# Optimization experiments

Hardware: AMD Instinct MI355X
Metric: run time of the kernel (lower is better)

Reference implementation:

```python
import jax, jax.numpy as jnp
import numpy as np

IN_CAP_NUM = 1024
IN_CAP_DIM = 64
OUT_CAP_NUM = 32
OUT_CAP_DIM = 64
BATCH = 64
NUM_ITER = 3


def squash(t):
    # t: [..., d]; scale = |t|^2 / (1+|t|^2) / |t|
    sq = jnp.sum(t * t, axis=-1, keepdims=True)
    scale = sq / (1.0 + sq) / jnp.sqrt(sq)
    return scale * t


def setup_inputs() -> dict:
    key = jax.random.key(0)
    k1, k2 = jax.random.split(key)
    x = jax.random.normal(k1, (IN_CAP_NUM, BATCH, IN_CAP_DIM), dtype=jnp.float32)
    route_w = 0.1 * jax.random.normal(
        k2, (OUT_CAP_NUM, IN_CAP_NUM, IN_CAP_DIM, OUT_CAP_DIM), dtype=jnp.float32)
    return {"x": x, "route_w": route_w}


def reference(x, route_w):
    # u[o,i,b,e] = sum_d x[i,b,d] * route_w[o,i,d,e]  (torch broadcast matmul)
    u = jnp.einsum('ibd,oide->oibe', x, route_w)  # [O, I, B, E]
    O = route_w.shape[0]
    b = jnp.zeros((O, 1, 1, 1), dtype=u.dtype)
    v = None
    for it in range(NUM_ITER):
        c = jax.nn.softmax(b, axis=0)                 # coupling over out caps
        s = jnp.sum(c * u, axis=1)                    # [O, B, E]
        v = squash(s)                                 # [O, B, E]
        if it < NUM_ITER - 1:
            # agreement: [O, I, B, 1]
            b = b + jnp.sum(u * v[:, None, :, :], axis=-1, keepdims=True)
    return v
```

## Files before the change

kernel.cpp:

```cpp
#include <hip/hip_runtime.h>
#include <hip/hip_bf16.h>
#include <stdint.h>


#define IC 1024
#define OC 32
#define DD 64
#define EE 64
#define BB 64

typedef __attribute__((ext_vector_type(8))) short short8;
typedef __attribute__((ext_vector_type(16))) float f32x16;

__device__ __forceinline__ unsigned short f2bf(float f) {
    unsigned int u = __float_as_uint(f);
    u = (u + 0x7FFFu + ((u >> 16) & 1u)) >> 16;
    return (unsigned short)u;
}
__device__ __forceinline__ unsigned int pk2(float a, float b) {
    return (unsigned int)f2bf(a) | ((unsigned int)f2bf(b) << 16);
}

template<bool UNIFORM>
__global__ __launch_bounds__(256)
void gemm_s_kernel(const float* __restrict__ x,
                   const float* __restrict__ w,
                   const float* __restrict__ cbuf,
                   float* __restrict__ s_out)
{
    __shared__ unsigned short xs[64 * 68];
    __shared__ unsigned short wT[64 * 68];
    const int t = threadIdx.x;
    const int o = blockIdx.y;
    const int chunk = blockIdx.x;
    const int lane = t & 63;
    const int wv = t >> 6;
    const int bh = wv & 1, eh = wv >> 1;
    const int seg = t & 7;
    const int rrow = t >> 3;

    f32x16 acc = (f32x16)0.0f;

    for (int ii = 0; ii < 32; ++ii) {
        const int i = chunk * 32 + ii;
        __syncthreads();
        for (int hlf = 0; hlf < 2; ++hlf) {
            const int b = rrow + hlf * 32;
            const float* xp = x + (((size_t)i) * BB + b) * DD + seg * 8;
            const float4 xa = *(const float4*)xp;
            const float4 xb = *(const float4*)(xp + 4);
            float c;
            if (UNIFORM) c = 1.0f / 32.0f;
            else         c = cbuf[(((size_t)o) * IC + i) * BB + b];
            uint2* dst = (uint2*)&xs[b * 68 + seg * 8];
            dst[0] = make_uint2(pk2(xa.x * c, xa.y * c), pk2(xa.z * c, xa.w * c));
            dst[1] = make_uint2(pk2(xb.x * c, xb.y * c), pk2(xb.z * c, xb.w * c));
        }
        {
            const int d0 = rrow * 2;
            const float* wp = w + ((((size_t)o) * IC + i) * DD + d0) * EE + seg * 8;
            const float4 a0 = *(const float4*)(wp);
            const float4 a1 = *(const float4*)(wp + 4);
            const float4 b0 = *(const float4*)(wp + EE);
            const float4 b1 = *(const float4*)(wp + EE + 4);
            const float r0[8] = {a0.x, a0.y, a0.z, a0.w, a1.x, a1.y, a1.z, a1.w};
            const float r1[8] = {b0.x, b0.y, b0.z, b0.w, b1.x, b1.y, b1.z, b1.w};
            #pragma unroll
            for (int j = 0; j < 8; ++j) {
                const int e = seg * 8 + j;
                *(unsigned int*)&wT[e * 68 + d0] = pk2(r0[j], r1[j]);
            }
        }
        __syncthreads();
        #pragma unroll
        for (int kk = 0; kk < 4; ++kk) {
            const int k0 = kk * 16 + (lane >> 5) * 8;
            const int ar = bh * 32 + (lane & 31);
            const int br = eh * 32 + (lane & 31);
            uint2 alo = *(const uint2*)&xs[ar * 68 + k0];
            uint2 ahi = *(const uint2*)&xs[ar * 68 + k0 + 4];
            uint2 blo = *(const uint2*)&wT[br * 68 + k0];
            uint2 bhi = *(const uint2*)&wT[br * 68 + k0 + 4];
            union { uint4 u; short8 s; } au, bu;
            au.u = make_uint4(alo.x, alo.y, ahi.x, ahi.y);
            bu.u = make_uint4(blo.x, blo.y, bhi.x, bhi.y);
            acc = __builtin_amdgcn_mfma_f32_32x32x16_bf16(au.s, bu.s, acc, 0, 0, 0);
        }
    }
    #pragma unroll
    for (int r = 0; r < 16; ++r) {
        const int gb = bh * 32 + (r & 3) + 8 * (r >> 2) + 4 * (lane >> 5);
        const int ge = eh * 32 + (lane & 31);
        atomicAdd(&s_out[(((size_t)o) * BB + gb) * EE + ge], acc[r]);
    }
}

template<bool FIRST>
__global__ __launch_bounds__(256)
void logits_kernel(const float* __restrict__ x,
                   const float* __restrict__ w,
                   const unsigned short* __restrict__ vbuf,
                   const float* __restrict__ bprev,
                   float* __restrict__ bout,
                   float* __restrict__ cbuf)
{
    __shared__ float xT[64 * 65];
    __shared__ unsigned short wls[64 * 68];
    __shared__ unsigned short vls[64 * 68];
    __shared__ float Lp[OC][2][BB];
    const int t = threadIdx.x;
    const int i = blockIdx.x;
    const int lane = t & 63;
    const int wv = t >> 6;
    const int dh = wv & 1, bh = wv >> 1;
    const int seg = t & 7;
    const int rrow = t >> 3;

    for (int hlf = 0; hlf < 2; ++hlf) {
        const int b = rrow + hlf * 32;
        const float* xp = x + (((size_t)i) * BB + b) * DD + seg * 8;
        const float4 xa = *(const float4*)xp;
        const float4 xb = *(const float4*)(xp + 4);
        const float xv[8] = {xa.x, xa.y, xa.z, xa.w, xb.x, xb.y, xb.z, xb.w};
        #pragma unroll
        for (int j = 0; j < 8; ++j)
            xT[(seg * 8 + j) * 65 + b] = xv[j];
    }

    for (int o = 0; o < OC; ++o) {
        __syncthreads();
        for (int hlf = 0; hlf < 2; ++hlf) {
            const int d = rrow + hlf * 32;
            const float* wp = w + ((((size_t)o) * IC + i) * DD + d) * EE + seg * 8;
            const float4 wa = *(const float4*)wp;
            const float4 wb = *(const float4*)(wp + 4);
            uint2* dst = (uint2*)&wls[d * 68 + seg * 8];
            dst[0] = make_uint2(pk2(wa.x, wa.y), pk2(wa.z, wa.w));
            dst[1] = make_uint2(pk2(wb.x, wb.y), pk2(wb.z, wb.w));
            const int b = d;
            const uint4 vr = *(const uint4*)(vbuf + (((size_t)o) * BB + b) * EE + seg * 8);
            uint2* vdst = (uint2*)&vls[b * 68 + seg * 8];
            vdst[0] = make_uint2(vr.x, vr.y);
            vdst[1] = make_uint2(vr.z, vr.w);
        }
        __syncthreads();
        f32x16 acc = (f32x16)0.0f;
        #pragma unroll
        for (int kk = 0; kk < 4; ++kk) {
            const int k0 = kk * 16 + (lane >> 5) * 8;
            const int dr = dh * 32 + (lane & 31);
            const int br = bh * 32 + (lane & 31);
            uint2 alo = *(const uint2*)&wls[dr * 68 + k0];
            uint2 ahi = *(const uint2*)&wls[dr * 68 + k0 + 4];
            uint2 blo = *(const uint2*)&vls[br * 68 + k0];
            uint2 bhi = *(const uint2*)&vls[br * 68 + k0 + 4];
            union { uint4 u; short8 s; } au, bu;
            au.u = make_uint4(alo.x, alo.y, ahi.x, ahi.y);
            bu.u = make_uint4(blo.x, blo.y, bhi.x, bhi.y);
            acc = __builtin_amdgcn_mfma_f32_32x32x16_bf16(au.s, bu.s, acc, 0, 0, 0);
        }
        float partial = 0.f;
        const int bcol = bh * 32 + (lane & 31);
        #pragma unroll
        for (int r = 0; r < 16; ++r) {
            const int d = dh * 32 + (r & 3) + 8 * (r >> 2) + 4 * (lane >> 5);
            partial += xT[d * 65 + bcol] * acc[r];
        }
        partial += __shfl_xor(partial, 32);
        if (lane < 32) Lp[o][dh][bcol] = partial;
    }
    __syncthreads();
    if (t < BB) {
        const int b = t;
        float lt[OC];
        float m = -1e30f;
        #pragma unroll
        for (int o = 0; o < OC; ++o) {
            float L = Lp[o][0][b] + Lp[o][1][b];
            if (!FIRST) L += bprev[(((size_t)o) * IC + i) * BB + b];
            if (FIRST)  bout[(((size_t)o) * IC + i) * BB + b] = L;
            lt[o] = L;
            m = fmaxf(m, L);
        }
        float Z = 0.f;
        #pragma unroll
        for (int o = 0; o < OC; ++o) { lt[o] = __expf(lt[o] - m); Z += lt[o]; }
        const float rZ = 1.0f / Z;
        #pragma unroll
        for (int o = 0; o < OC; ++o)
            cbuf[(((size_t)o) * IC + i) * BB + b] = lt[o] * rZ;
    }
}

template<bool TOBF>
__global__ __launch_bounds__(256)
void squash_kernel(const float* __restrict__ s, void* __restrict__ vout)
{
    const int o = blockIdx.x;
    const int lane = threadIdx.x & 63;
    const int wv = threadIdx.x >> 6;
    for (int b = wv; b < BB; b += 4) {
        const float val = s[(((size_t)o) * BB + b) * EE + lane];
        float sq = val * val;
        #pragma unroll
        for (int off = 1; off < 64; off <<= 1)
            sq += __shfl_xor(sq, off);
        const float r = sqrtf(sq);
        const float scale = r / (1.0f + sq);
        const size_t idx = (((size_t)o) * BB + b) * EE + lane;
        if (TOBF) ((unsigned short*)vout)[idx] = f2bf(val * scale);
        else      ((float*)vout)[idx] = val * scale;
    }
}

extern "C" void kernel_launch(void* const* d_in, const int* in_sizes, int n_in,
                              void* d_out, int out_size, void* d_ws, size_t ws_size,
                              hipStream_t stream)
{
    const float* x = (const float*)d_in[0];
    const float* w = (const float*)d_in[1];
    float* out = (float*)d_out;

    char* ws = (char*)d_ws;
    float*          s_buf = (float*)ws;
    unsigned short* vbuf  = (unsigned short*)(ws + 524288);
    float*          b1    = (float*)(ws + 524288 + 262144);
    float*          cbuf  = (float*)(ws + 524288 + 262144 + 8388608);

    const dim3 gridG(32, 32), blk(256);

    hipMemsetAsync(s_buf, 0, 524288, stream);
    gemm_s_kernel<true><<<gridG, blk, 0, stream>>>(x, w, nullptr, s_buf);
    squash_kernel<true><<<32, 256, 0, stream>>>(s_buf, vbuf);
    logits_kernel<true><<<1024, 256, 0, stream>>>(x, w, vbuf, nullptr, b1, cbuf);
    hipMemsetAsync(s_buf, 0, 524288, stream);
    gemm_s_kernel<false><<<gridG, blk, 0, stream>>>(x, w, cbuf, s_buf);
    squash_kernel<true><<<32, 256, 0, stream>>>(s_buf, vbuf);
    logits_kernel<false><<<1024, 256, 0, stream>>>(x, w, vbuf, b1, nullptr, cbuf);
    hipMemsetAsync(s_buf, 0, 524288, stream);
    gemm_s_kernel<false><<<gridG, blk, 0, stream>>>(x, w, cbuf, s_buf);
    squash_kernel<false><<<32, 256, 0, stream>>>(s_buf, out);
}
```

Measured before the change: 1.193 ms.

## Materialize u once in fp16 and reuse it across routing iterations

```diff
diff --git a/kernel.cpp b/kernel.cpp
--- a/kernel.cpp
+++ b/kernel.cpp
@@ -1,5 +1,4 @@
 #include <hip/hip_runtime.h>
-#include <hip/hip_bf16.h>
 #include <stdint.h>
 
 
@@ -11,6 +10,7 @@
 
 typedef __attribute__((ext_vector_type(8))) short short8;
 typedef __attribute__((ext_vector_type(16))) float f32x16;
+typedef _Float16 half8 __attribute__((ext_vector_type(8)));
 
 __device__ __forceinline__ unsigned short f2bf(float f) {
     unsigned int u = __float_as_uint(f);
@@ -21,11 +21,10 @@
     return (unsigned int)f2bf(a) | ((unsigned int)f2bf(b) << 16);
 }
 
-template<bool UNIFORM>
-__global__ __launch_bounds__(256)
-void gemm_s_kernel(const float* __restrict__ x,
+__global__ __launch_bounds__(256)
+void u_gemm_kernel(const float* __restrict__ x,
                    const float* __restrict__ w,
-                   const float* __restrict__ cbuf,
+                   _Float16* __restrict__ u,
                    float* __restrict__ s_out)
 {
     __shared__ unsigned short xs[64 * 68];
@@ -39,7 +38,7 @@
     const int seg = t & 7;
     const int rrow = t >> 3;
 
-    f32x16 acc = (f32x16)0.0f;
+    f32x16 stot = (f32x16)0.0f;
 
     for (int ii = 0; ii < 32; ++ii) {
         const int i = chunk * 32 + ii;
@@ -49,12 +48,9 @@
             const float* xp = x + (((size_t)i) * BB + b) * DD + seg * 8;
             const float4 xa = *(const float4*)xp;
             const float4 xb = *(const float4*)(xp + 4);
-            float c;
-            if (UNIFORM) c = 1.0f / 32.0f;
-            else         c = cbuf[(((size_t)o) * IC + i) * BB + b];
             uint2* dst = (uint2*)&xs[b * 68 + seg * 8];
-            dst[0] = make_uint2(pk2(xa.x * c, xa.y * c), pk2(xa.z * c, xa.w * c));
-            dst[1] = make_uint2(pk2(xb.x * c, xb.y * c), pk2(xb.z * c, xb.w * c));
+            dst[0] = make_uint2(pk2(xa.x, xa.y), pk2(xa.z, xa.w));
+            dst[1] = make_uint2(pk2(xb.x, xb.y), pk2(xb.z, xb.w));
         }
         {
             const int d0 = rrow * 2;
@@ -72,6 +68,7 @@
             }
         }
         __syncthreads();
+        f32x16 acc = (f32x16)0.0f;
         #pragma unroll
         for (int kk = 0; kk < 4; ++kk) {
             const int k0 = kk * 16 + (lane >> 5) * 8;
@@ -81,104 +78,69 @@
             uint2 ahi = *(const uint2*)&xs[ar * 68 + k0 + 4];
             uint2 blo = *(const uint2*)&wT[br * 68 + k0];
             uint2 bhi = *(const uint2*)&wT[br * 68 + k0 + 4];
-            union { uint4 u; short8 s; } au, bu;
-            au.u = make_uint4(alo.x, alo.y, ahi.x, ahi.y);
-            bu.u = make_uint4(blo.x, blo.y, bhi.x, bhi.y);
+            union { uint4 q; short8 s; } au, bu;
+            au.q = make_uint4(alo.x, alo.y, ahi.x, ahi.y);
+            bu.q = make_uint4(blo.x, blo.y, bhi.x, bhi.y);
             acc = __builtin_amdgcn_mfma_f32_32x32x16_bf16(au.s, bu.s, acc, 0, 0, 0);
+        }
+        _Float16* ub = u + ((((size_t)o) * IC + i) * BB) * EE;
+        #pragma unroll
+        for (int r = 0; r < 16; ++r) {
+            const int gb = bh * 32 + (r & 3) + 8 * (r >> 2) + 4 * (lane >> 5);
+            const int ge = eh * 32 + (lane & 31);
+            ub[gb * EE + ge] = (_Float16)acc[r];
+            stot[r] += acc[r];
         }
     }
     #pragma unroll
     for (int r = 0; r < 16; ++r) {
         const int gb = bh * 32 + (r & 3) + 8 * (r >> 2) + 4 * (lane >> 5);
         const int ge = eh * 32 + (lane & 31);
-        atomicAdd(&s_out[(((size_t)o) * BB + gb) * EE + ge], acc[r]);
+        atomicAdd(&s_out[(((size_t)o) * BB + gb) * EE + ge], stot[r] * (1.0f / 32.0f));
     }
 }
 
 template<bool FIRST>
 __global__ __launch_bounds__(256)
-void logits_kernel(const float* __restrict__ x,
-                   const float* __restrict__ w,
-                   const unsigned short* __restrict__ vbuf,
+void logits_kernel(const _Float16* __restrict__ u,
+                   const float* __restrict__ v,
                    const float* __restrict__ bprev,
                    float* __restrict__ bout,
                    float* __restrict__ cbuf)
 {
-    __shared__ float xT[64 * 65];
-    __shared__ unsigned short wls[64 * 68];
-    __shared__ unsigned short vls[64 * 68];
-    __shared__ float Lp[OC][2][BB];
+    __shared__ float Lp[OC][BB];
     const int t = threadIdx.x;
     const int i = blockIdx.x;
-    const int lane = t & 63;
-    const int wv = t >> 6;
-    const int dh = wv & 1, bh = wv >> 1;
-    const int seg = t & 7;
-    const int rrow = t >> 3;
-
-    for (int hlf = 0; hlf < 2; ++hlf) {
-        const int b = rrow + hlf * 32;
-        const float* xp = x + (((size_t)i) * BB + b) * DD + seg * 8;
-        const float4 xa = *(const float4*)xp;
-        const float4 xb = *(const float4*)(xp + 4);
-        const float xv[8] = {xa.x, xa.y, xa.z, xa.w, xb.x, xb.y, xb.z, xb.w};
-        #pragma unroll
-        for (int j = 0; j < 8; ++j)
-            xT[(seg * 8 + j) * 65 + b] = xv[j];
-    }
+    const int b = t >> 2;
+    const int eq = t & 3;
 
     for (int o = 0; o < OC; ++o) {
-        __syncthreads();
-        for (int hlf = 0; hlf < 2; ++hlf) {
-            const int d = rrow + hlf * 32;
-            const float* wp = w + ((((size_t)o) * IC + i) * DD + d) * EE + seg * 8;
-            const float4 wa = *(const float4*)wp;
-            const float4 wb = *(const float4*)(wp + 4);
-            uint2* dst = (uint2*)&wls[d * 68 + seg * 8];
-            dst[0] = make_uint2(pk2(wa.x, wa.y), pk2(wa.z, wa.w));
-            dst[1] = make_uint2(pk2(wb.x, wb.y), pk2(wb.z, wb.w));
-            const int b = d;
-            const uint4 vr = *(const uint4*)(vbuf + (((size_t)o) * BB + b) * EE + seg * 8);
-            uint2* vdst = (uint2*)&vls[b * 68 + seg * 8];
-            vdst[0] = make_uint2(vr.x, vr.y);
-            vdst[1] = make_uint2(vr.z, vr.w);
-        }
-        __syncthreads();
-        f32x16 acc = (f32x16)0.0f;
-        #pragma unroll
-        for (int kk = 0; kk < 4; ++kk) {
-            const int k0 = kk * 16 + (lane >> 5) * 8;
-            const int dr = dh * 32 + (lane & 31);
-            const int br = bh * 32 + (lane & 31);
-            uint2 alo = *(const uint2*)&wls[dr * 68 + k0];
-            uint2 ahi = *(const uint2*)&wls[dr * 68 + k0 + 4];
-            uint2 blo = *(const uint2*)&vls[br * 68 + k0];
-            uint2 bhi = *(const uint2*)&vls[br * 68 + k0 + 4];
-            union { uint4 u; short8 s; } au, bu;
-            au.u = make_uint4(alo.x, alo.y, ahi.x, ahi.y);
-            bu.u = make_uint4(blo.x, blo.y, bhi.x, bhi.y);
-            acc = __builtin_amdgcn_mfma_f32_32x32x16_bf16(au.s, bu.s, acc, 0, 0, 0);
-        }
-        float partial = 0.f;
-        const int bcol = bh * 32 + (lane & 31);
-        #pragma unroll
-        for (int r = 0; r < 16; ++r) {
-            const int d = dh * 32 + (r & 3) + 8 * (r >> 2) + 4 * (lane >> 5);
-            partial += xT[d * 65 + bcol] * acc[r];
-        }
-        partial += __shfl_xor(partial, 32);
-        if (lane < 32) Lp[o][dh][bcol] = partial;
+        const _Float16* up = u + ((((size_t)o) * IC + i) * BB + b) * EE + eq * 16;
+        const float*    vp = v + (((size_t)o) * BB + b) * EE + eq * 16;
+        const half8 u0 = *(const half8*)up;
+        const half8 u1 = *(const half8*)(up + 8);
+        const float4 va = *(const float4*)vp;
+        const float4 vb = *(const float4*)(vp + 4);
+        const float4 vc = *(const float4*)(vp + 8);
+        const float4 vd = *(const float4*)(vp + 12);
+        float p = (float)u0[0]*va.x + (float)u0[1]*va.y + (float)u0[2]*va.z + (float)u0[3]*va.w
+                + (float)u0[4]*vb.x + (float)u0[5]*vb.y + (float)u0[6]*vb.z + (float)u0[7]*vb.w
+                + (float)u1[0]*vc.x + (float)u1[1]*vc.y + (float)u1[2]*vc.z + (float)u1[3]*vc.w
+                + (float)u1[4]*vd.x + (float)u1[5]*vd.y + (float)u1[6]*vd.z + (float)u1[7]*vd.w;
+        p += __shfl_xor(p, 1);
+        p += __shfl_xor(p, 2);
+        if (eq == 0) Lp[o][b] = p;
     }
     __syncthreads();
     if (t < BB) {
-        const int b = t;
+        const int bb = t;
         float lt[OC];
         float m = -1e30f;
         #pragma unroll
         for (int o = 0; o < OC; ++o) {
-            float L = Lp[o][0][b] + Lp[o][1][b];
-            if (!FIRST) L += bprev[(((size_t)o) * IC + i) * BB + b];
-            if (FIRST)  bout[(((size_t)o) * IC + i) * BB + b] = L;
+            float L = Lp[o][bb];
+            if (!FIRST) L += bprev[(((size_t)o) * IC + i) * BB + bb];
+            if (FIRST)  bout[(((size_t)o) * IC + i) * BB + bb] = L;
             lt[o] = L;
             m = fmaxf(m, L);
         }
@@ -188,28 +150,55 @@
         const float rZ = 1.0f / Z;
         #pragma unroll
         for (int o = 0; o < OC; ++o)
-            cbuf[(((size_t)o) * IC + i) * BB + b] = lt[o] * rZ;
-    }
-}
-
-template<bool TOBF>
-__global__ __launch_bounds__(256)
-void squash_kernel(const float* __restrict__ s, void* __restrict__ vout)
+            cbuf[(((size_t)o) * IC + i) * BB + bb] = lt[o] * rZ;
+    }
+}
+
+__global__ __launch_bounds__(256)
+void sweight_kernel(const _Float16* __restrict__ u,
+                    const float* __restrict__ cbuf,
+                    float* __restrict__ s_out)
+{
+    const int t = threadIdx.x;
+    const int chunk = blockIdx.x;
+    const int o = blockIdx.y;
+    const int b = t >> 2;
+    const int eq = t & 3;
+    float acc[16];
+    #pragma unroll
+    for (int j = 0; j < 16; ++j) acc[j] = 0.f;
+    const int i0 = chunk * 32;
+    for (int ii = 0; ii < 32; ++ii) {
+        const int i = i0 + ii;
+        const float c = cbuf[(((size_t)o) * IC + i) * BB + b];
+        const _Float16* up = u + ((((size_t)o) * IC + i) * BB + b) * EE + eq * 16;
+        const half8 u0 = *(const half8*)up;
+        const half8 u1 = *(const half8*)(up + 8);
+        #pragma unroll
+        for (int j = 0; j < 8; ++j) acc[j]     += c * (float)u0[j];
+        #pragma unroll
+        for (int j = 0; j < 8; ++j) acc[8 + j] += c * (float)u1[j];
+    }
+    float* sp = s_out + (((size_t)o) * BB + b) * EE + eq * 16;
+    #pragma unroll
+    for (int j = 0; j < 16; ++j) atomicAdd(&sp[j], acc[j]);
+}
+
+__global__ __launch_bounds__(256)
+void squash_kernel(const float* __restrict__ s, float* __restrict__ vout)
 {
     const int o = blockIdx.x;
     const int lane = threadIdx.x & 63;
     const int wv = threadIdx.x >> 6;
     for (int b = wv; b < BB; b += 4) {
-        const float val = s[(((size_t)o) * BB + b) * EE + lane];
+        const size_t idx = (((size_t)o) * BB + b) * EE + lane;
+        const float val = s[idx];
         float sq = val * val;
         #pragma unroll
         for (int off = 1; off < 64; off <<= 1)
             sq += __shfl_xor(sq, off);
         const float r = sqrtf(sq);
-        const float scale = r / (1.0f + sq);
-        const size_t idx = (((size_t)o) * BB + b) * EE + lane;
-        if (TOBF) ((unsigned short*)vout)[idx] = f2bf(val * scale);
-        else      ((float*)vout)[idx] = val * scale;
+        vout[idx] = val * (r / (1.0f + sq));
     }
 }
 
@@ -222,22 +211,23 @@
     float* out = (float*)d_out;
 
     char* ws = (char*)d_ws;
-    float*          s_buf = (float*)ws;
-    unsigned short* vbuf  = (unsigned short*)(ws + 524288);
-    float*          b1    = (float*)(ws + 524288 + 262144);
-    float*          cbuf  = (float*)(ws + 524288 + 262144 + 8388608);
-
-    const dim3 gridG(32, 32), blk(256);
-
-    hipMemsetAsync(s_buf, 0, 524288, stream);
-    gemm_s_kernel<true><<<gridG, blk, 0, stream>>>(x, w, nullptr, s_buf);
-    squash_kernel<true><<<32, 256, 0, stream>>>(s_buf, vbuf);
-    logits_kernel<true><<<1024, 256, 0, stream>>>(x, w, vbuf, nullptr, b1, cbuf);
-    hipMemsetAsync(s_buf, 0, 524288, stream);
-    gemm_s_kernel<false><<<gridG, blk, 0, stream>>>(x, w, cbuf, s_buf);
-    squash_kernel<true><<<32, 256, 0, stream>>>(s_buf, vbuf);
-    logits_kernel<false><<<1024, 256, 0, stream>>>(x, w, vbuf, b1, nullptr, cbuf);
-    hipMemsetAsync(s_buf, 0, 524288, stream);
-    gemm_s_kernel<false><<<gridG, blk, 0, stream>>>(x, w, cbuf, s_buf);
-    squash_kernel<false><<<32, 256, 0, stream>>>(s_buf, out);
-}
+    float*    s_buf = (float*)ws;
+    float*    vbuf  = (float*)(ws + (1 << 19));
+    float*    b1    = (float*)(ws + (1 << 20));
+    float*    cbuf  = (float*)(ws + (1 << 20) + (8 << 20));
+    _Float16* u     = (_Float16*)(ws + (17u << 20));
+
+    const dim3 blk(256);
+
+    hipMemsetAsync(s_buf, 0, 1 << 19, stream);
+    u_gemm_kernel<<<dim3(32, 32), blk, 0, stream>>>(x, w, u, s_buf);
+    squash_kernel<<<32, blk, 0, stream>>>(s_buf, vbuf);
+    logits_kernel<true><<<1024, blk, 0, stream>>>(u, vbuf, nullptr, b1, cbuf);
+    hipMemsetAsync(s_buf, 0, 1 << 19, stream);
+    sweight_kernel<<<dim3(32, 32), blk, 0, stream>>>(u, cbuf, s_buf);
+    squash_kernel<<<32, blk, 0, stream>>>(s_buf, vbuf);
+    logits_kernel<false><<<1024, blk, 0, stream>>>(u, vbuf, b1, nullptr, cbuf);
+    hipMemsetAsync(s_buf, 0, 1 << 19, stream);
+    sweight_kernel<<<dim3(32, 32), blk, 0, stream>>>(u, cbuf, s_buf);
+    squash_kernel<<<32, blk, 0, stream>>>(s_buf, out);
+}
```

Result: slower. 1.415 ms (+18.7%).
